# Kernel optimization log

Hardware: AMD Instinct MI355X
Metric: run time of the kernel (lower is better)

## Reference

```python
import jax, jax.numpy as jnp
import numpy as np

K = 1024
D = 256
BETA = 0.25
DECAY = 0.99
EPS = 1e-05


def setup_inputs() -> dict:
    key = jax.random.key(0)
    k1, k2, k3, k4 = jax.random.split(key, 4)
    z_e = jax.random.normal(k1, (32, 2048, D), dtype=jnp.float32)
    emb = jax.random.normal(k2, (K, D), dtype=jnp.float32)
    # module L2-normalizes the codebook rows at init
    emb = emb / jnp.linalg.norm(emb, axis=1, keepdims=True)
    cluster_size = jax.random.uniform(k3, (K,), dtype=jnp.float32)
    embed_avg = jax.random.normal(k4, (K, D), dtype=jnp.float32)
    return {"z_e": z_e, "embedding": emb, "cluster_size": cluster_size, "embed_avg": embed_avg}


def reference(z_e, embedding, cluster_size, embed_avg):
    B, T, d = z_e.shape
    z = z_e.reshape(-1, d)                                   # [N, D]
    # squared-distance matrix: ||z||^2 - 2 z E^T + ||e||^2   -> [N, K]
    z_sq = jnp.sum(z * z, axis=1, keepdims=True)
    e_sq = jnp.sum(embedding * embedding, axis=1)[None, :]
    dist = z_sq - 2.0 * (z @ embedding.T) + e_sq
    codes = jnp.argmin(dist, axis=1)                         # [N]
    z_q = embedding[codes].reshape(z_e.shape)                # gather + reshape

    # ---- EMA codebook update (training branch, no-grad in torch) ----
    # scatter-reduce instead of materializing the [N, K] one-hot
    cs_batch = jax.ops.segment_sum(jnp.ones_like(codes, dtype=z.dtype), codes, num_segments=K)
    embed_sum = jax.ops.segment_sum(z, codes, num_segments=K)          # [K, D]
    new_cluster_size = cluster_size * DECAY + cs_batch * (1.0 - DECAY)
    new_embed_avg = embed_avg * DECAY + embed_sum * (1.0 - DECAY)
    n = jnp.sum(new_cluster_size)
    cs_smoothed = (new_cluster_size + EPS) / (n + K * EPS) * n
    new_embedding = new_embed_avg / cs_smoothed[:, None]

    commit_loss = jnp.mean((z_e - z_q) ** 2)
    vq_loss = BETA * commit_loss
    z_q_st = z_e + (z_q - z_e)  # straight-through (identical values in fwd)
    return (z_q_st, vq_loss, codes.reshape(B, T), new_embedding, new_cluster_size, new_embed_avg)
```

## Files before the change

### kernel.cpp

```cpp
#include <hip/hip_runtime.h>


#define DDIM 256
#define DQ   64
#define KC   1024
#define NROW 65536
#define BM   128
#define BN   128
#define BD   32
#define LS   34
#define DECAYF 0.99f
#define OMDF   0.01f
#define BETAF  0.25f
#define EPSF   1e-5f

typedef _Float16 f16;
typedef _Float16 f16x8 __attribute__((ext_vector_type(8)));
typedef float    f32x4 __attribute__((ext_vector_type(4)));

__device__ __forceinline__ void gl_lds16(const f16* g, f16* l) {
    __builtin_amdgcn_global_load_lds(
        (const __attribute__((address_space(1))) void*)g,
        (__attribute__((address_space(3))) void*)l, 16, 0, 0);
}

__global__ __launch_bounds__(256) void vq_esq(const float* __restrict__ emb,
                                              float* __restrict__ esq_g)
{
    int k = blockIdx.x * 256 + threadIdx.x;
    const float4* ep = (const float4*)(emb + (size_t)k * DDIM);
    float s = 0.f;
    for (int q = 0; q < DQ; ++q) {
        float4 v = ep[q];
        s += v.x * v.x + v.y * v.y + v.z * v.z + v.w * v.w;
    }
    esq_g[k] = s;
}

__global__ __launch_bounds__(256) void vq_prep(const float* __restrict__ src,
                                               f16* __restrict__ dst)
{
    int t   = blockIdx.x * 256 + threadIdx.x;
    int row = t >> 5;
    int c   = t & 31;
    int dc  = c >> 2, q = c & 3;
    const float4* sp = (const float4*)(src + (size_t)row * DDIM + c * 8);
    float4 v0 = sp[0], v1 = sp[1];
    float x[8] = {v0.x, v0.y, v0.z, v0.w, v1.x, v1.y, v1.z, v1.w};
    f16x8 h, l;
#pragma unroll
    for (int j = 0; j < 8; ++j) {
        float xs = x[j] * 128.0f;
        f16 hh = (f16)xs;
        h[j] = hh;
        l[j] = (f16)(xs - (float)hh);
    }
    f16* rp = dst + (size_t)row * 512 + dc * 64;
    *(f16x8*)(rp + q * 8)      = h;
    *(f16x8*)(rp + 32 + q * 8) = l;
}

__global__ __launch_bounds__(256) void vq_main_mfma(
    const float* __restrict__ z,
    const float* __restrict__ emb,
    const f16*  __restrict__ zhl,
    const f16*  __restrict__ ehl,
    const float* __restrict__ esq_g,
    float* __restrict__ out_zq,
    float* __restrict__ out_codes,
    float* __restrict__ loss_acc)
{
    __shared__ f16 As[8192];
    __shared__ f16 Bs[8192];
    __shared__ float esq_s[KC];
    __shared__ float zsq_s[BM];

    const int tid  = threadIdx.x;
    const int row0 = blockIdx.x * BM;

    {
        float4 v = ((const float4*)esq_g)[tid];
        *(float4*)(esq_s + tid * 4) = v;
    }
    if (tid < BM) {
        const float4* zp = (const float4*)(z + (size_t)(row0 + tid) * DDIM);
        float s = 0.f;
        for (int q = 0; q < DQ; ++q) {
            float4 v = zp[q];
            s += v.x * v.x + v.y * v.y + v.z * v.z + v.w * v.w;
        }
        zsq_s[tid] = s;
    }

    const f16* a_src[4];
    const f16* b_src[4];
    f16* a_dst[4];
    f16* b_dst[4];
#pragma unroll
    for (int i = 0; i < 4; ++i) {
        int s = tid + 256 * i;
        int r = s >> 3;
        int c = (s & 7) ^ (r & 7);
        a_src[i] = zhl + (size_t)(row0 + r) * 512 + c * 8;
        b_src[i] = ehl + (size_t)r * 512 + c * 8;
        a_dst[i] = As + s * 8;
        b_dst[i] = Bs + s * 8;
    }

    const int wave  = tid >> 6;
    const int lane  = tid & 63;
    const int wr    = wave >> 1, wc = wave & 1;
    const int row16 = lane & 15;
    const int kg    = lane >> 4;
    const int m     = row16 & 7;
    const int coh   = (kg ^ m) * 8;
    const int col_  = ((kg + 4) ^ m) * 8;
    int aoff[4], boff[4];
#pragma unroll
    for (int i = 0; i < 4; ++i) {
        aoff[i] = (wr * 64 + i * 16 + row16) * 64;
        boff[i] = (wc * 64 + i * 16 + row16) * 64;
    }

    __syncthreads();
    float zsqr[16];
#pragma unroll
    for (int i = 0; i < 4; ++i)
#pragma unroll
        for (int t = 0; t < 4; ++t)
            zsqr[i * 4 + t] = zsq_s[wr * 64 + i * 16 + kg * 4 + t];

    float runv[16];
    int   runi[16];
#pragma unroll
    for (int i = 0; i < 16; ++i) { runv[i] = 3.4e38f; runi[i] = 0; }

#pragma unroll 1
    for (int kt = 0; kt < KC / BN; ++kt) {
        f32x4 acc[4][4];
        f32x4 zero = {0.f, 0.f, 0.f, 0.f};
#pragma unroll
        for (int i = 0; i < 4; ++i)
#pragma unroll
            for (int j = 0; j < 4; ++j) acc[i][j] = zero;

#pragma unroll 1
        for (int dc = 0; dc < DDIM / BD; ++dc) {
            __syncthreads();
            int off = dc * 64;
            size_t bo = (size_t)kt * 65536 + off;
#pragma unroll
            for (int i = 0; i < 4; ++i) {
                gl_lds16(a_src[i] + off, a_dst[i]);
                gl_lds16(b_src[i] + bo,  b_dst[i]);
            }
            __syncthreads();

            f16x8 ah[4], al[4];
#pragma unroll
            for (int i = 0; i < 4; ++i) {
                ah[i] = *(const f16x8*)(As + aoff[i] + coh);
                al[i] = *(const f16x8*)(As + aoff[i] + col_);
            }
#pragma unroll
            for (int j = 0; j < 4; ++j) {
                f16x8 bh = *(const f16x8*)(Bs + boff[j] + coh);
                f16x8 bl = *(const f16x8*)(Bs + boff[j] + col_);
#pragma unroll
                for (int i = 0; i < 4; ++i) {
                    acc[i][j] = __builtin_amdgcn_mfma_f32_16x16x32_f16(ah[i], bh, acc[i][j], 0, 0, 0);
                    acc[i][j] = __builtin_amdgcn_mfma_f32_16x16x32_f16(ah[i], bl, acc[i][j], 0, 0, 0);
                    acc[i][j] = __builtin_amdgcn_mfma_f32_16x16x32_f16(al[i], bh, acc[i][j], 0, 0, 0);
                }
            }
        }

#pragma unroll
        for (int j = 0; j < 4; ++j) {
            int col = kt * BN + wc * 64 + j * 16 + row16;
            float es = esq_s[col];
#pragma unroll
            for (int i = 0; i < 4; ++i) {
#pragma unroll
                for (int t = 0; t < 4; ++t) {
                    float d = fmaf(acc[i][j][t], -0x1p-13f, zsqr[i * 4 + t]) + es;
                    if (d < runv[i * 4 + t]) { runv[i * 4 + t] = d; runi[i * 4 + t] = col; }
                }
            }
        }
    }

    __syncthreads();
    float* red_v = (float*)As;
    int*   red_i = (int*)Bs;
#pragma unroll
    for (int i = 0; i < 4; ++i)
#pragma unroll
        for (int t = 0; t < 4; ++t) {
            int lr = wr * 64 + i * 16 + kg * 4 + t;
            red_v[lr * 32 + wc * 16 + row16] = runv[i * 4 + t];
            red_i[lr * 32 + wc * 16 + row16] = runi[i * 4 + t];
        }
    __syncthreads();
    int* codes_s = (int*)zsq_s;
    if (tid < BM) {
        float bv = red_v[tid * 32];
        int   bi = red_i[tid * 32];
        for (int t = 1; t < 32; ++t) {
            float v  = red_v[tid * 32 + t];
            int   ix = red_i[tid * 32 + t];
            if (v < bv || (v == bv && ix < bi)) { bv = v; bi = ix; }
        }
        codes_s[tid] = bi;
        out_codes[row0 + tid] = (float)bi;
    }
    __syncthreads();

    float* lred = esq_s;
    float lp = 0.f;
    for (int r = wave; r < BM; r += 4) {
        int code = codes_s[r];
        float4 e4 = *(const float4*)(emb + (size_t)code * DDIM + lane * 4);
        float4 z4 = *(const float4*)(z + (size_t)(row0 + r) * DDIM + lane * 4);
        float dx = e4.x - z4.x, dy = e4.y - z4.y, dz = e4.z - z4.z, dw = e4.w - z4.w;
        float4 o;
        o.x = z4.x + dx; o.y = z4.y + dy; o.z = z4.z + dz; o.w = z4.w + dw;
        *(float4*)(out_zq + (size_t)(row0 + r) * DDIM + lane * 4) = o;
        lp += dx * dx + dy * dy + dz * dz + dw * dw;
    }
    lred[tid] = lp;
    __syncthreads();
    for (int s = 128; s > 0; s >>= 1) {
        if (tid < s) lred[tid] += lred[tid + s];
        __syncthreads();
    }
    if (tid == 0) atomicAdd(loss_acc, lred[0]);
}

__global__ __launch_bounds__(256) void vq_main_f32(
    const float* __restrict__ z,
    const float* __restrict__ emb,
    const float* __restrict__ esq_g,
    float* __restrict__ out_zq,
    float* __restrict__ out_codes,
    float* __restrict__ loss_acc)
{
    __shared__ float zs[BM * LS];
    __shared__ float es[BN * LS];
    __shared__ float esq_s[KC];
    __shared__ float zsq_s[BM];
    float* red_v   = zs;
    int*   red_i   = (int*)(zs + 2048);
    int*   codes_s = (int*)es;
    float* lred    = es + 128;

    const int tid  = threadIdx.x;
    const int row0 = blockIdx.x * BM;
    const int trow = tid >> 4;
    const int tcol = tid & 15;

    {
        const float4* eg = (const float4*)esq_g;
        float4 v = eg[tid];
        *(float4*)(esq_s + tid * 4) = v;
    }
    if (tid < BM) {
        const float4* zp = (const float4*)(z + (size_t)(row0 + tid) * DDIM);
        float s = 0.f;
        for (int q = 0; q < DQ; ++q) {
            float4 v = zp[q];
            s += v.x * v.x + v.y * v.y + v.z * v.z + v.w * v.w;
        }
        zsq_s[tid] = s;
    }

    const int r0 = tid >> 3;
    const int q0 = tid & 7;
    const float* zp0 = z + (size_t)(row0 + r0) * DDIM + q0 * 4;
    const float* ep0 = emb + (size_t)r0 * DDIM + q0 * 4;
    const int ls0 = r0 * LS + q0 * 4;

    float4 pz[4], pe[4];
#pragma unroll
    for (int it = 0; it < 4; ++it) {
        pz[it] = *(const float4*)(zp0 + it * 32 * DDIM);
        pe[it] = *(const float4*)(ep0 + it * 32 * DDIM);
    }

    float runv[8];
    int   runi[8];
#pragma unroll
    for (int i = 0; i < 8; ++i) { runv[i] = 3.4e38f; runi[i] = 0; }

#pragma unroll 1
    for (int kt = 0; kt < KC / BN; ++kt) {
        float acc[8][8];
#pragma unroll
        for (int i = 0; i < 8; ++i)
#pragma unroll
            for (int j = 0; j < 8; ++j) acc[i][j] = 0.f;

#pragma unroll 1
        for (int dc = 0; dc < DDIM / BD; ++dc) {
            __syncthreads();
#pragma unroll
            for (int it = 0; it < 4; ++it) {
                int o = ls0 + it * 32 * LS;
                *(float2*)(zs + o)     = make_float2(pz[it].x, pz[it].y);
                *(float2*)(zs + o + 2) = make_float2(pz[it].z, pz[it].w);
                *(float2*)(es + o)     = make_float2(pe[it].x, pe[it].y);
                *(float2*)(es + o + 2) = make_float2(pe[it].z, pe[it].w);
            }
            __syncthreads();
            {
                int ndc = dc + 1, nkt = kt;
                if (ndc == DDIM / BD) { ndc = 0; ++nkt; }
                if (nkt < KC / BN) {
                    size_t zo = (size_t)ndc * BD;
                    size_t eo = (size_t)nkt * BN * DDIM + (size_t)ndc * BD;
#pragma unroll
                    for (int it = 0; it < 4; ++it) {
                        pz[it] = *(const float4*)(zp0 + it * 32 * DDIM + zo);
                        pe[it] = *(const float4*)(ep0 + it * 32 * DDIM + eo);
                    }
                }
            }
#pragma unroll
            for (int s = 0; s < BD / 2; ++s) {
                float2 a2[8], b2[8];
#pragma unroll
                for (int i = 0; i < 8; ++i)
                    a2[i] = *(const float2*)(zs + (trow + 16 * i) * LS + s * 2);
#pragma unroll
                for (int j = 0; j < 8; ++j)
                    b2[j] = *(const float2*)(es + (tcol + 16 * j) * LS + s * 2);
#pragma unroll
                for (int i = 0; i < 8; ++i)
#pragma unroll
                    for (int j = 0; j < 8; ++j)
                        acc[i][j] = fmaf(a2[i].y, b2[j].y,
                                     fmaf(a2[i].x, b2[j].x, acc[i][j]));
            }
        }
#pragma unroll
        for (int i = 0; i < 8; ++i) {
            float zq2 = zsq_s[trow + 16 * i];
#pragma unroll
            for (int j = 0; j < 8; ++j) {
                int col = kt * BN + tcol + 16 * j;
                float dist = zq2 - 2.f * acc[i][j] + esq_s[col];
                if (dist < runv[i]) { runv[i] = dist; runi[i] = col; }
            }
        }
    }

    __syncthreads();
#pragma unroll
    for (int i = 0; i < 8; ++i) {
        int lr = trow + 16 * i;
        red_v[lr * 16 + tcol] = runv[i];
        red_i[lr * 16 + tcol] = runi[i];
    }
    __syncthreads();
    if (tid < BM) {
        float bv = red_v[tid * 16];
        int   bi = red_i[tid * 16];
        for (int t = 1; t < 16; ++t) {
            float v  = red_v[tid * 16 + t];
            int   ix = red_i[tid * 16 + t];
            if (v < bv || (v == bv && ix < bi)) { bv = v; bi = ix; }
        }
        codes_s[tid] = bi;
        out_codes[row0 + tid] = (float)bi;
    }
    __syncthreads();

    const int wavf = tid >> 6;
    const int lanf = tid & 63;
    float lp = 0.f;
    for (int r = wavf; r < BM; r += 4) {
        int code = codes_s[r];
        float4 e4 = *(const float4*)(emb + (size_t)code * DDIM + lanf * 4);
        float4 z4 = *(const float4*)(z + (size_t)(row0 + r) * DDIM + lanf * 4);
        float dx = e4.x - z4.x, dy = e4.y - z4.y, dz = e4.z - z4.z, dw = e4.w - z4.w;
        float4 o;
        o.x = z4.x + dx; o.y = z4.y + dy; o.z = z4.z + dz; o.w = z4.w + dw;
        *(float4*)(out_zq + (size_t)(row0 + r) * DDIM + lanf * 4) = o;
        lp += dx * dx + dy * dy + dz * dz + dw * dw;
    }
    lred[tid] = lp;
    __syncthreads();
    for (int s = 128; s > 0; s >>= 1) {
        if (tid < s) lred[tid] += lred[tid + s];
        __syncthreads();
    }
    if (tid == 0) atomicAdd(loss_acc, lred[0]);
}

__global__ __launch_bounds__(256) void vq_scatter(
    const float* __restrict__ z,
    const float* __restrict__ codes_f,
    float* __restrict__ embed_sum,
    float* __restrict__ counts)
{
    __shared__ int list[1024];
    __shared__ int nmatch;
    const int k   = blockIdx.x;
    const int tid = threadIdx.x;

    float acc = 0.f;
    int total = 0;
    if (tid == 0) nmatch = 0;
    __syncthreads();

    for (int base = 0; base < NROW; base += 1024) {
        float4 c4 = *(const float4*)(codes_f + base + tid * 4);
        int i0 = base + tid * 4;
        if ((int)c4.x == k) { int p = atomicAdd(&nmatch, 1); list[p] = i0; }
        if ((int)c4.y == k) { int p = atomicAdd(&nmatch, 1); list[p] = i0 + 1; }
        if ((int)c4.z == k) { int p = atomicAdd(&nmatch, 1); list[p] = i0 + 2; }
        if ((int)c4.w == k) { int p = atomicAdd(&nmatch, 1); list[p] = i0 + 3; }
        __syncthreads();
        int nm = nmatch;
        for (int i = 0; i < nm; ++i)
            acc += z[(size_t)list[i] * DDIM + tid];
        total += nm;
        __syncthreads();
        if (tid == 0) nmatch = 0;
        __syncthreads();
    }
    embed_sum[(size_t)k * DDIM + tid] = acc;
    if (tid == 0) counts[k] = (float)total;
}

__global__ void vq_finalize(const float* __restrict__ cluster_size,
                            const float* __restrict__ counts,
                            const float* __restrict__ loss_acc,
                            float* __restrict__ out_ncs,
                            float* __restrict__ out_loss,
                            float* __restrict__ cs_sm,
                            float inv_ND)
{
    __shared__ float sred[KC];
    const int tid = threadIdx.x;
    float ncs = cluster_size[tid] * DECAYF + counts[tid] * OMDF;
    out_ncs[tid] = ncs;
    sred[tid] = ncs;
    __syncthreads();
    for (int s = KC / 2; s > 0; s >>= 1) {
        if (tid < s) sred[tid] += sred[tid + s];
        __syncthreads();
    }
    float n = sred[0];
    cs_sm[tid] = (ncs + EPSF) / (n + (float)KC * EPSF) * n;
    if (tid == 0) out_loss[0] = BETAF * loss_acc[0] * inv_ND;
}

__global__ void vq_embed(const float* __restrict__ embed_avg,
                         const float* __restrict__ embed_sum,
                         const float* __restrict__ cs_sm,
                         float* __restrict__ out_nea,
                         float* __restrict__ out_nemb)
{
    int idx = blockIdx.x * blockDim.x + threadIdx.x;
    int k = idx >> 6;
    float4 ea = ((const float4*)embed_avg)[idx];
    float4 s4 = ((const float4*)embed_sum)[idx];
    float4 nea;
    nea.x = ea.x * DECAYF + s4.x * OMDF;
    nea.y = ea.y * DECAYF + s4.y * OMDF;
    nea.z = ea.z * DECAYF + s4.z * OMDF;
    nea.w = ea.w * DECAYF + s4.w * OMDF;
    ((float4*)out_nea)[idx] = nea;
    float cs = cs_sm[k];
    float4 ne;
    ne.x = nea.x / cs; ne.y = nea.y / cs; ne.z = nea.z / cs; ne.w = nea.w / cs;
    ((float4*)out_nemb)[idx] = ne;
}

extern "C" void kernel_launch(void* const* d_in, const int* in_sizes, int n_in,
                              void* d_out, int out_size, void* d_ws, size_t ws_size,
                              hipStream_t stream) {
    const float* z            = (const float*)d_in[0];
    const float* emb          = (const float*)d_in[1];
    const float* cluster_size = (const float*)d_in[2];
    const float* embed_avg    = (const float*)d_in[3];

    const int ND = in_sizes[0];
    const int KD = in_sizes[1];
    const int K  = in_sizes[2];
    const int N  = ND / DDIM;

    float* out       = (float*)d_out;
    float* out_zq    = out;
    float* out_loss  = out + (size_t)ND;
    float* out_codes = out + (size_t)ND + 1;
    float* out_nemb  = out + (size_t)ND + 1 + N;
    float* out_ncs   = out_nemb + (size_t)KD;
    float* out_nea   = out_ncs + (size_t)K;

    float* ws        = (float*)d_ws;
    float* loss_acc  = ws;
    float* counts    = ws + 1;
    float* cs_sm     = counts + K;
    float* esq_g     = cs_sm + K;
    float* embed_sum = esq_g + K;

    size_t base_floats = (size_t)1 + 3 * (size_t)K + (size_t)KD;
    size_t f16_off = (base_floats * sizeof(float) + 255) & ~(size_t)255;
    size_t zbytes  = (size_t)N * 512 * sizeof(f16);
    size_t ebytes  = (size_t)K * 512 * sizeof(f16);
    bool mfma_ok   = ws_size >= f16_off + zbytes + ebytes;

    hipMemsetAsync(loss_acc, 0, sizeof(float), stream);
    vq_esq<<<K / 256, 256, 0, stream>>>(emb, esq_g);
    if (mfma_ok) {
        f16* zhl = (f16*)((char*)d_ws + f16_off);
        f16* ehl = (f16*)((char*)d_ws + f16_off + zbytes);
        vq_prep<<<(N * 32) / 256, 256, 0, stream>>>(z, zhl);
        vq_prep<<<(K * 32) / 256, 256, 0, stream>>>(emb, ehl);
        vq_main_mfma<<<N / BM, 256, 0, stream>>>(z, emb, zhl, ehl, esq_g,
                                                 out_zq, out_codes, loss_acc);
    } else {
        vq_main_f32<<<N / BM, 256, 0, stream>>>(z, emb, esq_g,
                                                out_zq, out_codes, loss_acc);
    }
    vq_scatter<<<K, 256, 0, stream>>>(z, out_codes, embed_sum, counts);
    vq_finalize<<<1, K, 0, stream>>>(cluster_size, counts, loss_acc,
                                     out_ncs, out_loss, cs_sm, 1.0f / (float)ND);
    vq_embed<<<KD / 1024, 256, 0, stream>>>(embed_avg, embed_sum, cs_sm,
                                            out_nea, out_nemb);
}
```

Measured before the change: 337.5 us.

## Triple-buffer MFMA distance GEMM with larger row tiles and fused norm prep

```diff
diff --git a/kernel.cpp b/kernel.cpp
--- a/kernel.cpp
+++ b/kernel.cpp
@@ -14,6 +14,14 @@
 #define BETAF  0.25f
 #define EPSF   1e-5f
 
+#define BMR  256
+#define BNC  128
+#define NT8  8
+#define KST  12
+#define ABUF 16384
+#define BBUF 8192
+#define SMEM_BYTES (3*ABUF*2 + 3*BBUF*2 + 4096)
+
 typedef _Float16 f16;
 typedef _Float16 f16x8 __attribute__((ext_vector_type(8)));
 typedef float    f32x4 __attribute__((ext_vector_type(4)));
@@ -38,177 +46,200 @@
 }
 
 __global__ __launch_bounds__(256) void vq_prep(const float* __restrict__ src,
-                                               f16* __restrict__ dst)
+                                               f16* __restrict__ dst,
+                                               float* __restrict__ sq_g)
 {
     int t   = blockIdx.x * 256 + threadIdx.x;
     int row = t >> 5;
     int c   = t & 31;
-    int dc  = c >> 2, q = c & 3;
     const float4* sp = (const float4*)(src + (size_t)row * DDIM + c * 8);
     float4 v0 = sp[0], v1 = sp[1];
     float x[8] = {v0.x, v0.y, v0.z, v0.w, v1.x, v1.y, v1.z, v1.w};
     f16x8 h, l;
+    float s = 0.f;
 #pragma unroll
     for (int j = 0; j < 8; ++j) {
         float xs = x[j] * 128.0f;
         f16 hh = (f16)xs;
         h[j] = hh;
         l[j] = (f16)(xs - (float)hh);
-    }
-    f16* rp = dst + (size_t)row * 512 + dc * 64;
-    *(f16x8*)(rp + q * 8)      = h;
-    *(f16x8*)(rp + 32 + q * 8) = l;
-}
-
-__global__ __launch_bounds__(256) void vq_main_mfma(
+        s += x[j] * x[j];
+    }
+    f16* rp = dst + (size_t)row * 512;
+    *(f16x8*)(rp + c * 8)       = h;
+    *(f16x8*)(rp + 256 + c * 8) = l;
+    s += __shfl_xor(s, 1);
+    s += __shfl_xor(s, 2);
+    s += __shfl_xor(s, 4);
+    s += __shfl_xor(s, 8);
+    s += __shfl_xor(s, 16);
+    if (c == 0) sq_g[row] = s;
+}
+
+#define STAGE9(s_, nt_, b_) do {                                           \
+    int grp_ = (s_) >> 2, sm_ = (s_) & 3;                                  \
+    int ao_ = ((grp_ == 2) ? 256 : 0) + sm_ * 64;                          \
+    int bo_ = ((grp_ == 1) ? 256 : 0) + sm_ * 64;                          \
+    f16* ad_ = Al + (b_) * ABUF + tid * 8;                                 \
+    const f16* as_ = asrc0 + ao_;                                          \
+    gl_lds16(as_,             ad_);                                        \
+    gl_lds16(as_ +  64 * 512, ad_ + 4096);                                 \
+    gl_lds16(as_ + 128 * 512, ad_ + 8192);                                 \
+    gl_lds16(as_ + 192 * 512, ad_ + 12288);                                \
+    f16* bd_ = Bl + (b_) * BBUF + tid * 8;                                 \
+    const f16* bs_ = bsrc0 + (size_t)(nt_) * 65536 + bo_;                  \
+    gl_lds16(bs_,            bd_);                                         \
+    gl_lds16(bs_ + 64 * 512, bd_ + 4096);                                  \
+} while (0)
+
+__global__ __launch_bounds__(512) void vq_main_mfma(
     const float* __restrict__ z,
     const float* __restrict__ emb,
     const f16*  __restrict__ zhl,
     const f16*  __restrict__ ehl,
     const float* __restrict__ esq_g,
+    const float* __restrict__ zsq_g,
     float* __restrict__ out_zq,
     float* __restrict__ out_codes,
     float* __restrict__ loss_acc)
 {
-    __shared__ f16 As[8192];
-    __shared__ f16 Bs[8192];
-    __shared__ float esq_s[KC];
-    __shared__ float zsq_s[BM];
+    extern __shared__ f16 smem[];
+    f16* Al = smem;
+    f16* Bl = smem + 3 * ABUF;
+    float* esq_s = (float*)(smem + 3 * ABUF + 3 * BBUF);
 
     const int tid  = threadIdx.x;
-    const int row0 = blockIdx.x * BM;
-
-    {
-        float4 v = ((const float4*)esq_g)[tid];
-        *(float4*)(esq_s + tid * 4) = v;
-    }
-    if (tid < BM) {
-        const float4* zp = (const float4*)(z + (size_t)(row0 + tid) * DDIM);
-        float s = 0.f;
-        for (int q = 0; q < DQ; ++q) {
-            float4 v = zp[q];
-            s += v.x * v.x + v.y * v.y + v.z * v.z + v.w * v.w;
-        }
-        zsq_s[tid] = s;
-    }
-
-    const f16* a_src[4];
-    const f16* b_src[4];
-    f16* a_dst[4];
-    f16* b_dst[4];
-#pragma unroll
-    for (int i = 0; i < 4; ++i) {
-        int s = tid + 256 * i;
-        int r = s >> 3;
-        int c = (s & 7) ^ (r & 7);
-        a_src[i] = zhl + (size_t)(row0 + r) * 512 + c * 8;
-        b_src[i] = ehl + (size_t)r * 512 + c * 8;
-        a_dst[i] = As + s * 8;
-        b_dst[i] = Bs + s * 8;
-    }
-
-    const int wave  = tid >> 6;
-    const int lane  = tid & 63;
-    const int wr    = wave >> 1, wc = wave & 1;
-    const int row16 = lane & 15;
-    const int kg    = lane >> 4;
-    const int m     = row16 & 7;
-    const int coh   = (kg ^ m) * 8;
-    const int col_  = ((kg + 4) ^ m) * 8;
-    int aoff[4], boff[4];
-#pragma unroll
-    for (int i = 0; i < 4; ++i) {
-        aoff[i] = (wr * 64 + i * 16 + row16) * 64;
-        boff[i] = (wc * 64 + i * 16 + row16) * 64;
-    }
-
-    __syncthreads();
+    const int row0 = blockIdx.x * BMR;
+    const int wave = tid >> 6, lane = tid & 63;
+    const int wr = wave >> 1, wc = wave & 1;
+    const int row16 = lane & 15, kg = lane >> 4;
+
+    { float2 v = ((const float2*)esq_g)[tid];
+      *(float2*)(esq_s + tid * 2) = v; }
+
     float zsqr[16];
 #pragma unroll
     for (int i = 0; i < 4; ++i)
 #pragma unroll
         for (int t = 0; t < 4; ++t)
-            zsqr[i * 4 + t] = zsq_s[wr * 64 + i * 16 + kg * 4 + t];
-
-    float runv[16];
-    int   runi[16];
-#pragma unroll
-    for (int i = 0; i < 16; ++i) { runv[i] = 3.4e38f; runi[i] = 0; }
+            zsqr[i * 4 + t] = zsq_g[row0 + wr * 64 + i * 16 + kg * 4 + t];
+#pragma unroll
+    for (int q = 0; q < 16; ++q) asm volatile("" :: "v"(zsqr[q]));
+
+    const int arow = tid >> 3;
+    const int axor = ((tid & 7) ^ (arow & 7)) * 8;
+    const f16* asrc0 = zhl + (size_t)(row0 + arow) * 512 + axor;
+    const f16* bsrc0 = ehl + (size_t)arow * 512 + axor;
+
+    int aofs[4][2], bofs[4][2];
+#pragma unroll
+    for (int i = 0; i < 4; ++i)
+#pragma unroll
+        for (int kk = 0; kk < 2; ++kk) {
+            int ra = wr * 64 + i * 16 + row16;
+            aofs[i][kk] = ra * 64 + (((kk * 4 + kg) ^ (ra & 7)) * 8);
+            int rb = wc * 64 + i * 16 + row16;
+            bofs[i][kk] = rb * 64 + (((kk * 4 + kg) ^ (rb & 7)) * 8);
+        }
+
+    STAGE9(0, 0, 0);
+    STAGE9(1, 0, 1);
+    asm volatile("s_waitcnt lgkmcnt(0)" ::: "memory");
+    asm volatile("s_waitcnt vmcnt(6)" ::: "memory");
+    __builtin_amdgcn_s_barrier();
+
+    float runv[16]; int runi[16];
+#pragma unroll
+    for (int q = 0; q < 16; ++q) { runv[q] = 3.4e38f; runi[q] = 0; }
+
+    int s2 = 2, nt2 = 0, b2 = 2, bc = 0;
 
 #pragma unroll 1
-    for (int kt = 0; kt < KC / BN; ++kt) {
+    for (int nt = 0; nt < NT8; ++nt) {
         f32x4 acc[4][4];
-        f32x4 zero = {0.f, 0.f, 0.f, 0.f};
+        f32x4 zero4 = {0.f, 0.f, 0.f, 0.f};
 #pragma unroll
         for (int i = 0; i < 4; ++i)
 #pragma unroll
-            for (int j = 0; j < 4; ++j) acc[i][j] = zero;
+            for (int j = 0; j < 4; ++j) acc[i][j] = zero4;
 
 #pragma unroll 1
-        for (int dc = 0; dc < DDIM / BD; ++dc) {
-            __syncthreads();
-            int off = dc * 64;
-            size_t bo = (size_t)kt * 65536 + off;
-#pragma unroll
-            for (int i = 0; i < 4; ++i) {
-                gl_lds16(a_src[i] + off, a_dst[i]);
-                gl_lds16(b_src[i] + bo,  b_dst[i]);
+        for (int s = 0; s < KST; ++s) {
+            STAGE9(s2, nt2, b2);
+            ++s2; if (s2 == KST) { s2 = 0; ++nt2; if (nt2 == NT8) nt2 = 0; }
+            ++b2; if (b2 == 3) b2 = 0;
+
+            const f16* Ab = Al + bc * ABUF;
+            const f16* Bb = Bl + bc * BBUF;
+            __builtin_amdgcn_s_setprio(1);
+#pragma unroll
+            for (int kk = 0; kk < 2; ++kk) {
+                f16x8 af0 = *(const f16x8*)(Ab + aofs[0][kk]);
+                f16x8 af1 = *(const f16x8*)(Ab + aofs[1][kk]);
+                f16x8 af2 = *(const f16x8*)(Ab + aofs[2][kk]);
+                f16x8 af3 = *(const f16x8*)(Ab + aofs[3][kk]);
+                f16x8 bf0 = *(const f16x8*)(Bb + bofs[0][kk]);
+                f16x8 bf1 = *(const f16x8*)(Bb + bofs[1][kk]);
+                f16x8 bf2 = *(const f16x8*)(Bb + bofs[2][kk]);
+                f16x8 bf3 = *(const f16x8*)(Bb + bofs[3][kk]);
+                acc[0][0] = __builtin_amdgcn_mfma_f32_16x16x32_f16(af0, bf0, acc[0][0], 0, 0, 0);
+                acc[1][0] = __builtin_amdgcn_mfma_f32_16x16x32_f16(af1, bf0, acc[1][0], 0, 0, 0);
+                acc[2][0] = __builtin_amdgcn_mfma_f32_16x16x32_f16(af2, bf0, acc[2][0], 0, 0, 0);
+                acc[3][0] = __builtin_amdgcn_mfma_f32_16x16x32_f16(af3, bf0, acc[3][0], 0, 0, 0);
+                acc[0][1] = __builtin_amdgcn_mfma_f32_16x16x32_f16(af0, bf1, acc[0][1], 0, 0, 0);
+                acc[1][1] = __builtin_amdgcn_mfma_f32_16x16x32_f16(af1, bf1, acc[1][1], 0, 0, 0);
+                acc[2][1] = __builtin_amdgcn_mfma_f32_16x16x32_f16(af2, bf1, acc[2][1], 0, 0, 0);
+                acc[3][1] = __builtin_amdgcn_mfma_f32_16x16x32_f16(af3, bf1, acc[3][1], 0, 0, 0);
+                acc[0][2] = __builtin_amdgcn_mfma_f32_16x16x32_f16(af0, bf2, acc[0][2], 0, 0, 0);
+                acc[1][2] = __builtin_amdgcn_mfma_f32_16x16x32_f16(af1, bf2, acc[1][2], 0, 0, 0);
+                acc[2][2] = __builtin_amdgcn_mfma_f32_16x16x32_f16(af2, bf2, acc[2][2], 0, 0, 0);
+                acc[3][2] = __builtin_amdgcn_mfma_f32_16x16x32_f16(af3, bf2, acc[3][2], 0, 0, 0);
+                acc[0][3] = __builtin_amdgcn_mfma_f32_16x16x32_f16(af0, bf3, acc[0][3], 0, 0, 0);
+                acc[1][3] = __builtin_amdgcn_mfma_f32_16x16x32_f16(af1, bf3, acc[1][3], 0, 0, 0);
+                acc[2][3] = __builtin_amdgcn_mfma_f32_16x16x32_f16(af2, bf3, acc[2][3], 0, 0, 0);
+                acc[3][3] = __builtin_amdgcn_mfma_f32_16x16x32_f16(af3, bf3, acc[3][3], 0, 0, 0);
             }
-            __syncthreads();
-
-            f16x8 ah[4], al[4];
-#pragma unroll
-            for (int i = 0; i < 4; ++i) {
-                ah[i] = *(const f16x8*)(As + aoff[i] + coh);
-                al[i] = *(const f16x8*)(As + aoff[i] + col_);
-            }
-#pragma unroll
-            for (int j = 0; j < 4; ++j) {
-                f16x8 bh = *(const f16x8*)(Bs + boff[j] + coh);
-                f16x8 bl = *(const f16x8*)(Bs + boff[j] + col_);
-#pragma unroll
-                for (int i = 0; i < 4; ++i) {
-                    acc[i][j] = __builtin_amdgcn_mfma_f32_16x16x32_f16(ah[i], bh, acc[i][j], 0, 0, 0);
-                    acc[i][j] = __builtin_amdgcn_mfma_f32_16x16x32_f16(ah[i], bl, acc[i][j], 0, 0, 0);
-                    acc[i][j] = __builtin_amdgcn_mfma_f32_16x16x32_f16(al[i], bh, acc[i][j], 0, 0, 0);
-                }
-            }
+            __builtin_amdgcn_s_setprio(0);
+            ++bc; if (bc == 3) bc = 0;
+            asm volatile("s_waitcnt vmcnt(6)" ::: "memory");
+            __builtin_amdgcn_s_barrier();
         }
 
 #pragma unroll
         for (int j = 0; j < 4; ++j) {
-            int col = kt * BN + wc * 64 + j * 16 + row16;
+            int col = nt * BNC + wc * 64 + j * 16 + row16;
             float es = esq_s[col];
 #pragma unroll
-            for (int i = 0; i < 4; ++i) {
+            for (int i = 0; i < 4; ++i)
 #pragma unroll
                 for (int t = 0; t < 4; ++t) {
                     float d = fmaf(acc[i][j][t], -0x1p-13f, zsqr[i * 4 + t]) + es;
                     if (d < runv[i * 4 + t]) { runv[i * 4 + t] = d; runi[i * 4 + t] = col; }
                 }
-            }
-        }
-    }
-
-    __syncthreads();
-    float* red_v = (float*)As;
-    int*   red_i = (int*)Bs;
+        }
+    }
+
+    __syncthreads();
+    float* red_v = (float*)Al;
+    int*   red_i = (int*)((float*)Al + 32 * 258);
 #pragma unroll
     for (int i = 0; i < 4; ++i)
 #pragma unroll
         for (int t = 0; t < 4; ++t) {
-            int lr = wr * 64 + i * 16 + kg * 4 + t;
-            red_v[lr * 32 + wc * 16 + row16] = runv[i * 4 + t];
-            red_i[lr * 32 + wc * 16 + row16] = runi[i * 4 + t];
-        }
-    __syncthreads();
-    int* codes_s = (int*)zsq_s;
-    if (tid < BM) {
-        float bv = red_v[tid * 32];
-        int   bi = red_i[tid * 32];
+            int r = wr * 64 + i * 16 + kg * 4 + t;
+            int c = wc * 16 + row16;
+            red_v[c * 258 + r] = runv[i * 4 + t];
+            red_i[c * 258 + r] = runi[i * 4 + t];
+        }
+    __syncthreads();
+    int* codes_s = (int*)Bl;
+    if (tid < BMR) {
+        float bv = red_v[tid];
+        int   bi = red_i[tid];
+#pragma unroll 1
         for (int t = 1; t < 32; ++t) {
-            float v  = red_v[tid * 32 + t];
-            int   ix = red_i[tid * 32 + t];
+            float v  = red_v[t * 258 + tid];
+            int   ix = red_i[t * 258 + tid];
             if (v < bv || (v == bv && ix < bi)) { bv = v; bi = ix; }
         }
         codes_s[tid] = bi;
@@ -216,9 +247,10 @@
     }
     __syncthreads();
 
-    float* lred = esq_s;
+    float* lred = (float*)Bl + 256;
     float lp = 0.f;
-    for (int r = wave; r < BM; r += 4) {
+#pragma unroll 1
+    for (int r = wave; r < BMR; r += 8) {
         int code = codes_s[r];
         float4 e4 = *(const float4*)(emb + (size_t)code * DDIM + lane * 4);
         float4 z4 = *(const float4*)(z + (size_t)(row0 + r) * DDIM + lane * 4);
@@ -230,8 +262,8 @@
     }
     lred[tid] = lp;
     __syncthreads();
-    for (int s = 128; s > 0; s >>= 1) {
-        if (tid < s) lred[tid] += lred[tid + s];
+    for (int st = 256; st > 0; st >>= 1) {
+        if (tid < st) lred[tid] += lred[tid + st];
         __syncthreads();
     }
     if (tid == 0) atomicAdd(loss_acc, lred[0]);
@@ -504,24 +536,32 @@
     float* counts    = ws + 1;
     float* cs_sm     = counts + K;
     float* esq_g     = cs_sm + K;
-    float* embed_sum = esq_g + K;
-
-    size_t base_floats = (size_t)1 + 3 * (size_t)K + (size_t)KD;
+    float* zsq_g     = esq_g + K;
+    float* embed_sum = zsq_g + N;
+
+    size_t base_floats = (size_t)1 + 3 * (size_t)K + (size_t)N + (size_t)KD;
     size_t f16_off = (base_floats * sizeof(float) + 255) & ~(size_t)255;
     size_t zbytes  = (size_t)N * 512 * sizeof(f16);
     size_t ebytes  = (size_t)K * 512 * sizeof(f16);
     bool mfma_ok   = ws_size >= f16_off + zbytes + ebytes;
 
     hipMemsetAsync(loss_acc, 0, sizeof(float), stream);
-    vq_esq<<<K / 256, 256, 0, stream>>>(emb, esq_g);
     if (mfma_ok) {
+        static bool attr_done = false;
+        if (!attr_done) {
+            hipFuncSetAttribute((const void*)vq_main_mfma,
+                                hipFuncAttributeMaxDynamicSharedMemorySize,
+                                SMEM_BYTES);
+            attr_done = true;
+        }
         f16* zhl = (f16*)((char*)d_ws + f16_off);
         f16* ehl = (f16*)((char*)d_ws + f16_off + zbytes);
-        vq_prep<<<(N * 32) / 256, 256, 0, stream>>>(z, zhl);
-        vq_prep<<<(K * 32) / 256, 256, 0, stream>>>(emb, ehl);
-        vq_main_mfma<<<N / BM, 256, 0, stream>>>(z, emb, zhl, ehl, esq_g,
-                                                 out_zq, out_codes, loss_acc);
+        vq_prep<<<(N * 32) / 256, 256, 0, stream>>>(z, zhl, zsq_g);
+        vq_prep<<<(K * 32) / 256, 256, 0, stream>>>(emb, ehl, esq_g);
+        vq_main_mfma<<<N / BMR, 512, SMEM_BYTES, stream>>>(
+            z, emb, zhl, ehl, esq_g, zsq_g, out_zq, out_codes, loss_acc);
     } else {
+        vq_esq<<<K / 256, 256, 0, stream>>>(emb, esq_g);
         vq_main_f32<<<N / BM, 256, 0, stream>>>(z, emb, esq_g,
                                                 out_zq, out_codes, loss_acc);
     }
```

Result: faster. 321.1 us (-4.9%).
